# Kernel optimization log

Measured on AMD Instinct MI355X. Metric: run time of the kernel, lower is better.

The kernel has to match this reference:

```python
import jax, jax.numpy as jnp
import numpy as np
import math

B, S, I, C = 1, 512, 512, 256   # batch, n_seqs, n_res, c_in
H, D = 8, 32                    # num_heads, head_dim; total_dim = H*D = 256
TD = H * D


def setup_inputs() -> dict:
    key = jax.random.key(0)
    ks = jax.random.split(key, 12)
    w = lambda k, shape: (jax.random.normal(k, shape, dtype=jnp.float32) * 0.02)
    msa_representation = jax.random.normal(ks[0], (B, S, I, C), dtype=jnp.float32)
    msa_mask = (jax.random.uniform(ks[1], (B, S, I)) > 0.1).astype(jnp.float32)
    return {
        "msa_representation": msa_representation,
        "msa_mask": msa_mask,
        "ln_gamma": jnp.ones((C,), jnp.float32),
        "ln_beta": jnp.zeros((C,), jnp.float32),
        "Wq": w(ks[2], (C, TD)),
        "Wk": w(ks[3], (C, D)),
        "Wv": w(ks[4], (C, D)),
        "Wg": w(ks[5], (C, TD)),
        "bg": jnp.ones((TD,), jnp.float32),   # gate bias init = 1 (init_gate_linear)
        "Wo": w(ks[6], (TD, C)),
        "bo": jnp.zeros((C,), jnp.float32),
    }


def _layer_norm(x, gamma, beta, eps=1e-5):
    mu = jnp.mean(x, axis=-1, keepdims=True)
    var = jnp.mean(jnp.square(x - mu), axis=-1, keepdims=True)
    return (x - mu) * jax.lax.rsqrt(var + eps) * gamma + beta


def reference(msa_representation, msa_mask, ln_gamma, ln_beta,
              Wq, Wk, Wv, Wg, bg, Wo, bo):
    b, s, i, _ = msa_representation.shape
    x_ln = _layer_norm(msa_representation, ln_gamma, ln_beta)

    # Shared (head-less) K, V: [b, s, i, D]
    K = jnp.einsum('bsic,cd->bsid', x_ln, Wk)
    V = jnp.einsum('bsic,cd->bsid', x_ln, Wv)

    # Per-head query: [b, s, i, H, D]
    Q_si = jnp.einsum('bsic,ce->bsie', x_ln, Wq).reshape(b, s, i, H, D)

    # Masked mean-pool of the query over the sequence axis s -> [b, i, H, D]
    qm = msa_mask[..., None, None]                       # [b, s, i, 1, 1]
    Q = (Q_si * qm).sum(axis=1) / jnp.clip(qm.sum(axis=1), 1.0, None)

    # Sigmoid gate: [b, s, i, H, D]
    G = jax.nn.sigmoid(jnp.einsum('bsic,ce->bsie', x_ln, Wg) + bg).reshape(b, s, i, H, D)

    # Scores over the sequence axis t: [b, t, i, H]
    scores = jnp.einsum('bihc,btic->btih', Q, K) / math.sqrt(D)
    scores = scores + (1.0 - msa_mask[:, :, :, None]) * (-1e9)
    attention = jax.nn.softmax(scores, axis=1)

    # Weighted sum of shared V: [b, i, H, D], broadcast over s via gating
    weighted = jnp.einsum('btih,btic->bihc', attention, V)[:, None]  # [b,1,i,H,D]
    gated = (G * weighted).reshape(b, s, i, TD)
    output = jnp.einsum('bsie,ec->bsic', gated, Wo) + bo
    output = output * msa_mask[..., None]
    return output
```

## Files before the change

### kernel.cpp

```cpp
#include <hip/hip_runtime.h>

typedef __bf16 bf16_t;
typedef __bf16 bf16x4 __attribute__((ext_vector_type(4)));
typedef __bf16 bf16x8 __attribute__((ext_vector_type(8)));
typedef float f32x4 __attribute__((ext_vector_type(4)));

#define LXS 264

#define GLOAD_LDS16(gsrc, ldst) \
    __builtin_amdgcn_global_load_lds((__attribute__((address_space(1))) void*)(gsrc), \
                                     (__attribute__((address_space(3))) void*)(ldst), 16, 0, 0)

__global__ __launch_bounds__(256) void k_prep(
    const float* __restrict__ Wg, const float* __restrict__ Wo,
    const float* __restrict__ Wk, const float* __restrict__ Wv,
    bf16_t* __restrict__ WgP, bf16_t* __restrict__ WoP, bf16_t* __restrict__ WKVP)
{
    int id = blockIdx.x * 256 + threadIdx.x;
    if (id < 65536) {
        int j = id & 7, l = (id >> 3) & 63, kt = (id >> 9) & 7, nt = id >> 12;
        int k = kt * 32 + (l >> 4) * 8 + j;
        int n = nt * 16 + (l & 15);
        WgP[id] = (bf16_t)Wg[k * 256 + n];
    } else if (id < 131072) {
        int t = id - 65536;
        int j = t & 7, l = (t >> 3) & 63, kt = (t >> 9) & 7, nt = t >> 12;
        int k = kt * 32 + (l >> 4) * 8 + j;
        int n = nt * 16 + (l & 15);
        WoP[t] = (bf16_t)Wo[k * 256 + n];
    } else if (id < 147456) {
        int t = id - 131072;
        int j = t & 7, l = (t >> 3) & 63, kt = (t >> 9) & 7, nt = t >> 12;
        int k = kt * 32 + (l >> 4) * 8 + j;
        int n = nt * 16 + (l & 15);
        WKVP[t] = (bf16_t)(n < 32 ? Wk[k * 32 + n] : Wv[k * 32 + (n - 32)]);
    }
}

__global__ __launch_bounds__(256) void kA(
    const float* __restrict__ msa, const float* __restrict__ mask,
    const float* __restrict__ gamma, const float* __restrict__ beta,
    bf16_t* __restrict__ xln, bf16_t* __restrict__ kv, const bf16_t* __restrict__ WKVP,
    float* __restrict__ Qpart, float* __restrict__ Qcnt)
{
    __shared__ __align__(16) bf16_t lx[64 * LXS];
    __shared__ float pp[4][256];
    __shared__ float cw[4];
    int tid = threadIdx.x;
    int lane = tid & 63, w = tid >> 6;
    int l15 = lane & 15, l4 = lane >> 4;
    int i = blockIdx.x & 511;
    int schunk = blockIdx.x >> 9;
    int s0 = schunk * 64;

    float4 g4 = ((const float4*)gamma)[lane];
    float4 b4 = ((const float4*)beta)[lane];

    bf16x8 bfr[8];
    #pragma unroll
    for (int kt = 0; kt < 8; ++kt)
        bfr[kt] = *(const bf16x8*)(WKVP + ((w * 8 + kt) * 64 + lane) * 8);

    float p0 = 0, p1 = 0, p2 = 0, p3 = 0, pc = 0;
    for (int t = 0; t < 16; ++t) {
        int rl = w * 16 + t;
        size_t r = (size_t)(s0 + rl) * 512 + i;
        float4 x = ((const float4*)(msa + r * 256))[lane];
        float mv = mask[r];
        float s  = x.x + x.y + x.z + x.w;
        float ss = x.x*x.x + x.y*x.y + x.z*x.z + x.w*x.w;
        #pragma unroll
        for (int m = 32; m; m >>= 1) { s += __shfl_xor(s, m, 64); ss += __shfl_xor(ss, m, 64); }
        float mu = s * (1.0f / 256.0f);
        float var = ss * (1.0f / 256.0f) - mu * mu;
        float rs = rsqrtf(var + 1e-5f);
        float4 y;
        y.x = (x.x - mu) * rs * g4.x + b4.x;
        y.y = (x.y - mu) * rs * g4.y + b4.y;
        y.z = (x.z - mu) * rs * g4.z + b4.z;
        y.w = (x.w - mu) * rs * g4.w + b4.w;
        bf16x4 xv;
        xv[0] = (bf16_t)y.x; xv[1] = (bf16_t)y.y; xv[2] = (bf16_t)y.z; xv[3] = (bf16_t)y.w;
        *(bf16x4*)(xln + r * 256 + lane * 4) = xv;
        *(bf16x4*)(lx + rl * LXS + lane * 4) = xv;
        p0 += mv * y.x; p1 += mv * y.y; p2 += mv * y.z; p3 += mv * y.w;
        pc += mv;
    }
    *(float4*)&pp[w][lane * 4] = (float4){p0, p1, p2, p3};
    if (lane == 0) cw[w] = pc;
    __syncthreads();

    {
        float qs = pp[0][tid] + pp[1][tid] + pp[2][tid] + pp[3][tid];
        Qpart[((size_t)schunk * 512 + i) * 256 + tid] = qs;
        if (tid == 0) Qcnt[schunk * 512 + i] = cw[0] + cw[1] + cw[2] + cw[3];
    }

    f32x4 acc[4];
    #pragma unroll
    for (int rt = 0; rt < 4; ++rt) acc[rt] = (f32x4){0.f, 0.f, 0.f, 0.f};
    #pragma unroll
    for (int kt = 0; kt < 8; ++kt) {
        #pragma unroll
        for (int rt = 0; rt < 4; ++rt) {
            bf16x8 a = *(bf16x8*)(lx + (rt * 16 + l15) * LXS + kt * 32 + l4 * 8);
            acc[rt] = __builtin_amdgcn_mfma_f32_16x16x32_bf16(a, bfr[kt], acc[rt], 0, 0, 0);
        }
    }
    #pragma unroll
    for (int rt = 0; rt < 4; ++rt) {
        #pragma unroll
        for (int j = 0; j < 4; ++j) {
            int row = rt * 16 + l4 * 4 + j;
            size_t r = (size_t)(s0 + row) * 512 + i;
            kv[r * 64 + w * 16 + l15] = (bf16_t)acc[rt][j];
        }
    }
}

__global__ __launch_bounds__(256) void kB(
    const float* __restrict__ Qpart, const float* __restrict__ Qcnt,
    const float* __restrict__ Wq, float* __restrict__ Q)
{
    int i = blockIdx.x, tid = threadIdx.x;
    __shared__ float xs[256];
    float s = 0;
    #pragma unroll
    for (int ch = 0; ch < 8; ++ch) s += Qpart[((size_t)ch * 512 + i) * 256 + tid];
    xs[tid] = s;
    float cnt = 0;
    #pragma unroll
    for (int ch = 0; ch < 8; ++ch) cnt += Qcnt[ch * 512 + i];
    __syncthreads();
    float scale = 1.0f / (fmaxf(cnt, 1.0f) * 5.656854249492381f);
    float q = 0;
    for (int c = 0; c < 256; ++c) q += xs[c] * Wq[c * 256 + tid];
    Q[i * 256 + tid] = q * scale;
}

__global__ __launch_bounds__(256) void kC(
    const bf16_t* __restrict__ kv, const float* __restrict__ mask,
    const float* __restrict__ Q, float* __restrict__ wout)
{
    int i = blockIdx.x, tid = threadIdx.x;
    __shared__ __align__(16) bf16_t kbuf[512 * 32];
    __shared__ float sc[512 * 8];
    __shared__ float qq[256];
    __shared__ float mk[512];
    __shared__ float rcp[8];

    qq[tid] = Q[i * 256 + tid];
    mk[tid] = mask[tid * 512 + i];
    mk[tid + 256] = mask[(tid + 256) * 512 + i];

    for (int it = 0; it < 8; ++it) {
        int idx = it * 256 + tid; int t = idx >> 2; int q = idx & 3;
        ((uint4*)kbuf)[t * 4 + q] = ((const uint4*)kv)[((size_t)t * 512 + i) * 8 + q];
    }
    __syncthreads();

    for (int it = 0; it < 16; ++it) {
        int idx = it * 256 + tid; int t = idx >> 3; int h = idx & 7;
        float a = 0;
        #pragma unroll 8
        for (int d = 0; d < 32; ++d) a += qq[h * 32 + d] * (float)kbuf[t * 32 + d];
        sc[t * 8 + h] = a - (1.0f - mk[t]) * 1e9f;
    }
    __syncthreads();

    {
        int h = tid >> 5, l = tid & 31;
        float m = -1e30f;
        for (int k = 0; k < 16; ++k) m = fmaxf(m, sc[(l + 32 * k) * 8 + h]);
        #pragma unroll
        for (int off = 16; off; off >>= 1) m = fmaxf(m, __shfl_xor(m, off, 64));
        float s = 0;
        for (int k = 0; k < 16; ++k) {
            int idx = (l + 32 * k) * 8 + h;
            float p = __expf(sc[idx] - m);
            sc[idx] = p; s += p;
        }
        #pragma unroll
        for (int off = 16; off; off >>= 1) s += __shfl_xor(s, off, 64);
        if (l == 0) rcp[h] = 1.0f / s;
    }
    for (int it = 0; it < 8; ++it) {
        int idx = it * 256 + tid; int t = idx >> 2; int q = idx & 3;
        ((uint4*)kbuf)[t * 4 + q] = ((const uint4*)kv)[((size_t)t * 512 + i) * 8 + 4 + q];
    }
    __syncthreads();

    {
        int h = tid >> 5, d = tid & 31;
        float acc = 0;
        for (int t = 0; t < 512; ++t) acc += sc[t * 8 + h] * (float)kbuf[t * 32 + d];
        wout[i * 256 + tid] = acc * rcp[h];
    }
}

__global__ __launch_bounds__(256, 2) void kD(
    const bf16_t* __restrict__ xln, const bf16_t* __restrict__ WgP, const bf16_t* __restrict__ WoP,
    const float* __restrict__ bg, const float* __restrict__ bo,
    const float* __restrict__ weighted, const float* __restrict__ mask, float* __restrict__ out)
{
    __shared__ __align__(16) bf16_t lx[64 * 256];
    int tid = threadIdx.x;
    int lane = tid & 63, q = tid >> 6;
    int l15 = lane & 15, l4 = lane >> 4;
    int rowbase = blockIdx.x * 64;

    const bf16_t* srcBase = xln + (size_t)rowbase * 256;
    #pragma unroll
    for (int c = 0; c < 8; ++c) {
        int idx = (c * 256 + tid) * 16;
        int row = idx >> 9;
        int g = (idx >> 4) & 31;
        int gs = g ^ (row & 7);
        GLOAD_LDS16(srcBase + row * 256 + gs * 8, lx + c * 2048 + q * 512);
    }

    bf16x8 bfr[4][8];
    #pragma unroll
    for (int ctl = 0; ctl < 4; ++ctl)
        #pragma unroll
        for (int kt = 0; kt < 8; ++kt)
            bfr[ctl][kt] = *(const bf16x8*)(WgP + (((q * 4 + ctl) * 8 + kt) * 64 + lane) * 8);
    __syncthreads();

    int swb = l15 & 7;

    f32x4 acc[4][4];
    #pragma unroll
    for (int rt = 0; rt < 4; ++rt)
        #pragma unroll
        for (int ctl = 0; ctl < 4; ++ctl) acc[rt][ctl] = (f32x4){0.f, 0.f, 0.f, 0.f};

    #pragma unroll
    for (int kt = 0; kt < 8; ++kt) {
        bf16x8 a[4];
        #pragma unroll
        for (int rt = 0; rt < 4; ++rt)
            a[rt] = *(bf16x8*)(lx + (rt * 16 + l15) * 256 + ((kt * 4 + l4) ^ swb) * 8);
        #pragma unroll
        for (int ctl = 0; ctl < 4; ++ctl)
            #pragma unroll
            for (int rt = 0; rt < 4; ++rt)
                acc[rt][ctl] = __builtin_amdgcn_mfma_f32_16x16x32_bf16(a[rt], bfr[ctl][kt], acc[rt][ctl], 0, 0, 0);
    }
    __syncthreads();

    #pragma unroll
    for (int ctl = 0; ctl < 4; ++ctl)
        #pragma unroll
        for (int kt = 0; kt < 8; ++kt)
            bfr[ctl][kt] = *(const bf16x8*)(WoP + (((q * 4 + ctl) * 8 + kt) * 64 + lane) * 8);

    #pragma unroll
    for (int ctl = 0; ctl < 4; ++ctl) {
        int col = (q * 4 + ctl) * 16 + l15;
        float bgv = bg[col];
        int g0 = col >> 3, c7 = col & 7;
        #pragma unroll
        for (int rt = 0; rt < 4; ++rt) {
            #pragma unroll
            for (int j = 0; j < 4; ++j) {
                int row = rt * 16 + l4 * 4 + j;
                int i2 = (rowbase + row) & 511;
                float t = acc[rt][ctl][j] + bgv;
                float gv = 1.0f / (1.0f + __expf(-t));
                float gg = gv * weighted[i2 * 256 + col];
                lx[row * 256 + ((g0 ^ (row & 7)) << 3) + c7] = (bf16_t)gg;
            }
        }
    }
    __syncthreads();

    #pragma unroll
    for (int rt = 0; rt < 4; ++rt)
        #pragma unroll
        for (int ctl = 0; ctl < 4; ++ctl) acc[rt][ctl] = (f32x4){0.f, 0.f, 0.f, 0.f};
    #pragma unroll
    for (int kt = 0; kt < 8; ++kt) {
        bf16x8 a[4];
        #pragma unroll
        for (int rt = 0; rt < 4; ++rt)
            a[rt] = *(bf16x8*)(lx + (rt * 16 + l15) * 256 + ((kt * 4 + l4) ^ swb) * 8);
        #pragma unroll
        for (int ctl = 0; ctl < 4; ++ctl)
            #pragma unroll
            for (int rt = 0; rt < 4; ++rt)
                acc[rt][ctl] = __builtin_amdgcn_mfma_f32_16x16x32_bf16(a[rt], bfr[ctl][kt], acc[rt][ctl], 0, 0, 0);
    }
    #pragma unroll
    for (int ctl = 0; ctl < 4; ++ctl) {
        int col = (q * 4 + ctl) * 16 + l15;
        float bov = bo[col];
        #pragma unroll
        for (int rt = 0; rt < 4; ++rt) {
            #pragma unroll
            for (int j = 0; j < 4; ++j) {
                int row = rt * 16 + l4 * 4 + j;
                int r = rowbase + row;
                out[(size_t)r * 256 + col] = (acc[rt][ctl][j] + bov) * mask[r];
            }
        }
    }
}

extern "C" void kernel_launch(void* const* d_in, const int* in_sizes, int n_in,
                              void* d_out, int out_size, void* d_ws, size_t ws_size,
                              hipStream_t stream) {
    const float* msa   = (const float*)d_in[0];
    const float* mask  = (const float*)d_in[1];
    const float* gamma = (const float*)d_in[2];
    const float* beta  = (const float*)d_in[3];
    const float* Wq    = (const float*)d_in[4];
    const float* Wk    = (const float*)d_in[5];
    const float* Wv    = (const float*)d_in[6];
    const float* Wg    = (const float*)d_in[7];
    const float* bg    = (const float*)d_in[8];
    const float* Wo    = (const float*)d_in[9];
    const float* bo    = (const float*)d_in[10];
    float* out = (float*)d_out;

    char* ws = (char*)d_ws;
    bf16_t* xln   = (bf16_t*)(ws);
    bf16_t* kv    = (bf16_t*)(ws + 134217728);
    float*  Qp    = (float*)(ws + 167772160);
    float*  wgt   = (float*)(ws + 168296448);
    bf16_t* WgP   = (bf16_t*)(ws + 168820736);
    bf16_t* WoP   = (bf16_t*)(ws + 168951808);
    bf16_t* WKVP  = (bf16_t*)(ws + 169082880);
    float*  Qpart = (float*)(ws + 169115648);
    float*  Qcnt  = (float*)(ws + 173309952);

    k_prep<<<576, 256, 0, stream>>>(Wg, Wo, Wk, Wv, WgP, WoP, WKVP);
    kA<<<4096, 256, 0, stream>>>(msa, mask, gamma, beta, xln, kv, WKVP, Qpart, Qcnt);
    kB<<<512, 256, 0, stream>>>(Qpart, Qcnt, Wq, Qp);
    kC<<<512, 256, 0, stream>>>(kv, mask, Qp, wgt);
    kD<<<4096, 256, 0, stream>>>(xln, WgP, WoP, bg, bo, wgt, mask, out);
}
```

Before: 301.8 us.

## Make kD persistent over four row tiles with double-buffered LDS and vectorized epilogues

kD now processes four 64-row tiles per block, keeping the Wg B-fragments in registers across tiles and prefetching the next x_ln tile into a second LDS buffer while computing the current one. Wo fragments are streamed per k-step in a ping-pong fashion instead of all being held at once. MFMA operands are swapped so each lane owns four consecutive columns, which allows float4 and bf16x4 vectorized stores for the gate, the output and the kA kv write. This adds LDS usage (two 32KB buffers) and reduces grid size to 1024 blocks, which may lower occupancy and parallelism.

```diff
diff --git a/kernel.cpp b/kernel.cpp
--- a/kernel.cpp
+++ b/kernel.cpp
@@ -104,17 +104,17 @@
         #pragma unroll
         for (int rt = 0; rt < 4; ++rt) {
             bf16x8 a = *(bf16x8*)(lx + (rt * 16 + l15) * LXS + kt * 32 + l4 * 8);
-            acc[rt] = __builtin_amdgcn_mfma_f32_16x16x32_bf16(a, bfr[kt], acc[rt], 0, 0, 0);
+            acc[rt] = __builtin_amdgcn_mfma_f32_16x16x32_bf16(bfr[kt], a, acc[rt], 0, 0, 0);
         }
     }
     #pragma unroll
     for (int rt = 0; rt < 4; ++rt) {
-        #pragma unroll
-        for (int j = 0; j < 4; ++j) {
-            int row = rt * 16 + l4 * 4 + j;
-            size_t r = (size_t)(s0 + row) * 512 + i;
-            kv[r * 64 + w * 16 + l15] = (bf16_t)acc[rt][j];
-        }
+        int row = rt * 16 + l15;
+        size_t r = (size_t)(s0 + row) * 512 + i;
+        bf16x4 kvv;
+        #pragma unroll
+        for (int j = 0; j < 4; ++j) kvv[j] = (bf16_t)acc[rt][j];
+        *(bf16x4*)(kv + r * 64 + w * 16 + l4 * 4) = kvv;
     }
 }
 
@@ -203,108 +203,137 @@
     const float* __restrict__ bg, const float* __restrict__ bo,
     const float* __restrict__ weighted, const float* __restrict__ mask, float* __restrict__ out)
 {
-    __shared__ __align__(16) bf16_t lx[64 * 256];
+    __shared__ __align__(16) bf16_t lx0[64 * 256];
+    __shared__ __align__(16) bf16_t lx1[64 * 256];
     int tid = threadIdx.x;
     int lane = tid & 63, q = tid >> 6;
     int l15 = lane & 15, l4 = lane >> 4;
-    int rowbase = blockIdx.x * 64;
-
-    const bf16_t* srcBase = xln + (size_t)rowbase * 256;
-    #pragma unroll
-    for (int c = 0; c < 8; ++c) {
-        int idx = (c * 256 + tid) * 16;
-        int row = idx >> 9;
-        int g = (idx >> 4) & 31;
-        int gs = g ^ (row & 7);
-        GLOAD_LDS16(srcBase + row * 256 + gs * 8, lx + c * 2048 + q * 512);
-    }
-
-    bf16x8 bfr[4][8];
+    int swb = l15 & 7;
+
+#define STAGE(BUF, RB) \
+    { const bf16_t* sB = xln + (size_t)(RB) * 256; \
+      _Pragma("unroll") \
+      for (int c = 0; c < 8; ++c) { \
+        int idx = (c * 256 + tid) * 16; \
+        int row_ = idx >> 9; \
+        int g_ = (idx >> 4) & 31; \
+        GLOAD_LDS16(sB + row_ * 256 + (g_ ^ (row_ & 7)) * 8, (BUF) + c * 2048 + q * 512); \
+      } }
+
+#define LOAD_BO(DST, KT) \
+    _Pragma("unroll") \
+    for (int ctl = 0; ctl < 4; ++ctl) \
+        DST[ctl] = *(const bf16x8*)(WoP + ((((q * 4 + ctl) * 8 + (KT)) * 64 + lane) * 8));
+
+#define G2STEP(BO, KT, LXC) \
+    { bf16x8 a2[4]; \
+      _Pragma("unroll") \
+      for (int rt = 0; rt < 4; ++rt) \
+          a2[rt] = *(bf16x8*)((LXC) + (rt * 16 + l15) * 256 + (((KT) * 4 + l4) ^ swb) * 8); \
+      _Pragma("unroll") \
+      for (int ctl = 0; ctl < 4; ++ctl) \
+          _Pragma("unroll") \
+          for (int rt = 0; rt < 4; ++rt) \
+              acc[rt][ctl] = __builtin_amdgcn_mfma_f32_16x16x32_bf16(BO[ctl], a2[rt], acc[rt][ctl], 0, 0, 0); }
+
+    bf16x8 bfrG[4][8];
     #pragma unroll
     for (int ctl = 0; ctl < 4; ++ctl)
         #pragma unroll
         for (int kt = 0; kt < 8; ++kt)
-            bfr[ctl][kt] = *(const bf16x8*)(WgP + (((q * 4 + ctl) * 8 + kt) * 64 + lane) * 8);
-    __syncthreads();
-
-    int swb = l15 & 7;
+            bfrG[ctl][kt] = *(const bf16x8*)(WgP + (((q * 4 + ctl) * 8 + kt) * 64 + lane) * 8);
+
+    int Rblk = blockIdx.x * 256;
+    STAGE(lx0, Rblk)
+    __syncthreads();
 
     f32x4 acc[4][4];
-    #pragma unroll
-    for (int rt = 0; rt < 4; ++rt)
-        #pragma unroll
-        for (int ctl = 0; ctl < 4; ++ctl) acc[rt][ctl] = (f32x4){0.f, 0.f, 0.f, 0.f};
-
-    #pragma unroll
-    for (int kt = 0; kt < 8; ++kt) {
-        bf16x8 a[4];
+
+    #pragma unroll
+    for (int t = 0; t < 4; ++t) {
+        bf16_t* LXC = (t & 1) ? lx1 : lx0;
+        bf16_t* LXN = (t & 1) ? lx0 : lx1;
+        int R0 = Rblk + t * 64;
+
+        if (t < 3) STAGE(LXN, R0 + 64)
+
         #pragma unroll
         for (int rt = 0; rt < 4; ++rt)
-            a[rt] = *(bf16x8*)(lx + (rt * 16 + l15) * 256 + ((kt * 4 + l4) ^ swb) * 8);
-        #pragma unroll
-        for (int ctl = 0; ctl < 4; ++ctl)
+            #pragma unroll
+            for (int ctl = 0; ctl < 4; ++ctl) acc[rt][ctl] = (f32x4){0.f, 0.f, 0.f, 0.f};
+        #pragma unroll
+        for (int kt = 0; kt < 8; ++kt) {
+            bf16x8 a[4];
             #pragma unroll
             for (int rt = 0; rt < 4; ++rt)
-                acc[rt][ctl] = __builtin_amdgcn_mfma_f32_16x16x32_bf16(a[rt], bfr[ctl][kt], acc[rt][ctl], 0, 0, 0);
-    }
-    __syncthreads();
-
-    #pragma unroll
-    for (int ctl = 0; ctl < 4; ++ctl)
-        #pragma unroll
-        for (int kt = 0; kt < 8; ++kt)
-            bfr[ctl][kt] = *(const bf16x8*)(WoP + (((q * 4 + ctl) * 8 + kt) * 64 + lane) * 8);
-
-    #pragma unroll
-    for (int ctl = 0; ctl < 4; ++ctl) {
-        int col = (q * 4 + ctl) * 16 + l15;
-        float bgv = bg[col];
-        int g0 = col >> 3, c7 = col & 7;
-        #pragma unroll
-        for (int rt = 0; rt < 4; ++rt) {
-            #pragma unroll
-            for (int j = 0; j < 4; ++j) {
-                int row = rt * 16 + l4 * 4 + j;
-                int i2 = (rowbase + row) & 511;
-                float t = acc[rt][ctl][j] + bgv;
-                float gv = 1.0f / (1.0f + __expf(-t));
-                float gg = gv * weighted[i2 * 256 + col];
-                lx[row * 256 + ((g0 ^ (row & 7)) << 3) + c7] = (bf16_t)gg;
+                a[rt] = *(bf16x8*)(LXC + (rt * 16 + l15) * 256 + ((kt * 4 + l4) ^ swb) * 8);
+            #pragma unroll
+            for (int ctl = 0; ctl < 4; ++ctl)
+                #pragma unroll
+                for (int rt = 0; rt < 4; ++rt)
+                    acc[rt][ctl] = __builtin_amdgcn_mfma_f32_16x16x32_bf16(bfrG[ctl][kt], a[rt], acc[rt][ctl], 0, 0, 0);
+        }
+        __syncthreads();
+
+        #pragma unroll
+        for (int ctl = 0; ctl < 4; ++ctl) {
+            int c4 = (q * 4 + ctl) * 16 + l4 * 4;
+            float4 bg4 = *(const float4*)(bg + c4);
+            int g0 = c4 >> 3, c7 = c4 & 7;
+            #pragma unroll
+            for (int rt = 0; rt < 4; ++rt) {
+                int row = rt * 16 + l15;
+                int i2 = (R0 + row) & 511;
+                float4 w4 = *(const float4*)(weighted + i2 * 256 + c4);
+                f32x4 t4 = acc[rt][ctl];
+                bf16x4 gv;
+                gv[0] = (bf16_t)(w4.x / (1.0f + __expf(-(t4[0] + bg4.x))));
+                gv[1] = (bf16_t)(w4.y / (1.0f + __expf(-(t4[1] + bg4.y))));
+                gv[2] = (bf16_t)(w4.z / (1.0f + __expf(-(t4[2] + bg4.z))));
+                gv[3] = (bf16_t)(w4.w / (1.0f + __expf(-(t4[3] + bg4.w))));
+                *(bf16x4*)(LXC + row * 256 + ((g0 ^ (row & 7)) << 3) + c7) = gv;
             }
         }
-    }
-    __syncthreads();
-
-    #pragma unroll
-    for (int rt = 0; rt < 4; ++rt)
-        #pragma unroll
-        for (int ctl = 0; ctl < 4; ++ctl) acc[rt][ctl] = (f32x4){0.f, 0.f, 0.f, 0.f};
-    #pragma unroll
-    for (int kt = 0; kt < 8; ++kt) {
-        bf16x8 a[4];
+        __syncthreads();
+
         #pragma unroll
         for (int rt = 0; rt < 4; ++rt)
-            a[rt] = *(bf16x8*)(lx + (rt * 16 + l15) * 256 + ((kt * 4 + l4) ^ swb) * 8);
-        #pragma unroll
-        for (int ctl = 0; ctl < 4; ++ctl)
-            #pragma unroll
-            for (int rt = 0; rt < 4; ++rt)
-                acc[rt][ctl] = __builtin_amdgcn_mfma_f32_16x16x32_bf16(a[rt], bfr[ctl][kt], acc[rt][ctl], 0, 0, 0);
-    }
-    #pragma unroll
-    for (int ctl = 0; ctl < 4; ++ctl) {
-        int col = (q * 4 + ctl) * 16 + l15;
-        float bov = bo[col];
-        #pragma unroll
-        for (int rt = 0; rt < 4; ++rt) {
-            #pragma unroll
-            for (int j = 0; j < 4; ++j) {
-                int row = rt * 16 + l4 * 4 + j;
-                int r = rowbase + row;
-                out[(size_t)r * 256 + col] = (acc[rt][ctl][j] + bov) * mask[r];
+            #pragma unroll
+            for (int ctl = 0; ctl < 4; ++ctl) acc[rt][ctl] = (f32x4){0.f, 0.f, 0.f, 0.f};
+        {
+            bf16x8 boA[4], boB[4];
+            LOAD_BO(boA, 0)
+            LOAD_BO(boB, 1) G2STEP(boA, 0, LXC)
+            LOAD_BO(boA, 2) G2STEP(boB, 1, LXC)
+            LOAD_BO(boB, 3) G2STEP(boA, 2, LXC)
+            LOAD_BO(boA, 4) G2STEP(boB, 3, LXC)
+            LOAD_BO(boB, 5) G2STEP(boA, 4, LXC)
+            LOAD_BO(boA, 6) G2STEP(boB, 5, LXC)
+            LOAD_BO(boB, 7) G2STEP(boA, 6, LXC)
+                            G2STEP(boB, 7, LXC)
+        }
+
+        #pragma unroll
+        for (int ctl = 0; ctl < 4; ++ctl) {
+            int c4 = (q * 4 + ctl) * 16 + l4 * 4;
+            float4 bo4 = *(const float4*)(bo + c4);
+            #pragma unroll
+            for (int rt = 0; rt < 4; ++rt) {
+                int r = R0 + rt * 16 + l15;
+                float mv = mask[r];
+                float4 o;
+                o.x = (acc[rt][ctl][0] + bo4.x) * mv;
+                o.y = (acc[rt][ctl][1] + bo4.y) * mv;
+                o.z = (acc[rt][ctl][2] + bo4.z) * mv;
+                o.w = (acc[rt][ctl][3] + bo4.w) * mv;
+                *(float4*)(out + (size_t)r * 256 + c4) = o;
             }
         }
-    }
+        __syncthreads();
+    }
+#undef STAGE
+#undef LOAD_BO
+#undef G2STEP
 }
 
 extern "C" void kernel_launch(void* const* d_in, const int* in_sizes, int n_in,
@@ -338,5 +367,5 @@
     kA<<<4096, 256, 0, stream>>>(msa, mask, gamma, beta, xln, kv, WKVP, Qpart, Qcnt);
     kB<<<512, 256, 0, stream>>>(Qpart, Qcnt, Wq, Qp);
     kC<<<512, 256, 0, stream>>>(kv, mask, Qp, wgt);
-    kD<<<4096, 256, 0, stream>>>(xln, WgP, WoP, bg, bo, wgt, mask, out);
-}
+    kD<<<1024, 256, 0, stream>>>(xln, WgP, WoP, bg, bo, wgt, mask, out);
+}
```

Result: slower. 402.4 us (+33.3%).

## Move gate projection into the layernorm kernel and store sigmoid gate instead of xln

Applied to the files above, without the earlier changes.

The gate GEMM (x_ln·Wg plus bias and sigmoid) now runs in kA while the layer-normed tile is still in LDS, and the bf16 gate G is written in place of x_ln. kD becomes a register-only kernel: it loads G rows, multiplies by the attention-weighted values, and does the Wo GEMM with weights streamed from global, using non-temporal output stores and no LDS. The goal is to drop the x_ln round-trip and the LDS staging and synchronisation in kD. In exchange kA does much more MFMA work and holds more registers, and kD reloads WoP from global in every wave.

```diff
diff --git a/kernel.cpp b/kernel.cpp
--- a/kernel.cpp
+++ b/kernel.cpp
@@ -6,10 +6,6 @@
 typedef float f32x4 __attribute__((ext_vector_type(4)));
 
 #define LXS 264
-
-#define GLOAD_LDS16(gsrc, ldst) \
-    __builtin_amdgcn_global_load_lds((__attribute__((address_space(1))) void*)(gsrc), \
-                                     (__attribute__((address_space(3))) void*)(ldst), 16, 0, 0)
 
 __global__ __launch_bounds__(256) void k_prep(
     const float* __restrict__ Wg, const float* __restrict__ Wo,
@@ -40,7 +36,9 @@
 __global__ __launch_bounds__(256) void kA(
     const float* __restrict__ msa, const float* __restrict__ mask,
     const float* __restrict__ gamma, const float* __restrict__ beta,
-    bf16_t* __restrict__ xln, bf16_t* __restrict__ kv, const bf16_t* __restrict__ WKVP,
+    const float* __restrict__ bg,
+    bf16_t* __restrict__ G, bf16_t* __restrict__ kv,
+    const bf16_t* __restrict__ WKVP, const bf16_t* __restrict__ WgP,
     float* __restrict__ Qpart, float* __restrict__ Qcnt)
 {
     __shared__ __align__(16) bf16_t lx[64 * LXS];
@@ -81,7 +79,6 @@
         y.w = (x.w - mu) * rs * g4.w + b4.w;
         bf16x4 xv;
         xv[0] = (bf16_t)y.x; xv[1] = (bf16_t)y.y; xv[2] = (bf16_t)y.z; xv[3] = (bf16_t)y.w;
-        *(bf16x4*)(xln + r * 256 + lane * 4) = xv;
         *(bf16x4*)(lx + rl * LXS + lane * 4) = xv;
         p0 += mv * y.x; p1 += mv * y.y; p2 += mv * y.z; p3 += mv * y.w;
         pc += mv;
@@ -96,24 +93,70 @@
         if (tid == 0) Qcnt[schunk * 512 + i] = cw[0] + cw[1] + cw[2] + cw[3];
     }
 
-    f32x4 acc[4];
-    #pragma unroll
-    for (int rt = 0; rt < 4; ++rt) acc[rt] = (f32x4){0.f, 0.f, 0.f, 0.f};
-    #pragma unroll
-    for (int kt = 0; kt < 8; ++kt) {
+    {
+        f32x4 acc[4];
+        #pragma unroll
+        for (int rt = 0; rt < 4; ++rt) acc[rt] = (f32x4){0.f, 0.f, 0.f, 0.f};
+        #pragma unroll
+        for (int kt = 0; kt < 8; ++kt) {
+            #pragma unroll
+            for (int rt = 0; rt < 4; ++rt) {
+                bf16x8 a = *(bf16x8*)(lx + (rt * 16 + l15) * LXS + kt * 32 + l4 * 8);
+                acc[rt] = __builtin_amdgcn_mfma_f32_16x16x32_bf16(bfr[kt], a, acc[rt], 0, 0, 0);
+            }
+        }
         #pragma unroll
         for (int rt = 0; rt < 4; ++rt) {
-            bf16x8 a = *(bf16x8*)(lx + (rt * 16 + l15) * LXS + kt * 32 + l4 * 8);
-            acc[rt] = __builtin_amdgcn_mfma_f32_16x16x32_bf16(a, bfr[kt], acc[rt], 0, 0, 0);
-        }
-    }
-    #pragma unroll
-    for (int rt = 0; rt < 4; ++rt) {
-        #pragma unroll
-        for (int j = 0; j < 4; ++j) {
-            int row = rt * 16 + l4 * 4 + j;
+            int row = rt * 16 + l15;
             size_t r = (size_t)(s0 + row) * 512 + i;
-            kv[r * 64 + w * 16 + l15] = (bf16_t)acc[rt][j];
+            bf16x4 kvv;
+            #pragma unroll
+            for (int j = 0; j < 4; ++j) kvv[j] = (bf16_t)acc[rt][j];
+            *(bf16x4*)(kv + r * 64 + w * 16 + l4 * 4) = kvv;
+        }
+    }
+
+    #pragma unroll
+    for (int cp = 0; cp < 2; ++cp) {
+        int nt0 = w * 4 + cp * 2, nt1 = nt0 + 1;
+        f32x4 ga0[4], ga1[4];
+        #pragma unroll
+        for (int rt = 0; rt < 4; ++rt) { ga0[rt] = (f32x4){0.f,0.f,0.f,0.f}; ga1[rt] = (f32x4){0.f,0.f,0.f,0.f}; }
+        bf16x8 w0 = *(const bf16x8*)(WgP + ((nt0 * 8 + 0) * 64 + lane) * 8);
+        bf16x8 w1 = *(const bf16x8*)(WgP + ((nt1 * 8 + 0) * 64 + lane) * 8);
+        #pragma unroll
+        for (int kt = 0; kt < 8; ++kt) {
+            int ktn = (kt + 1) & 7;
+            bf16x8 w0n = *(const bf16x8*)(WgP + ((nt0 * 8 + ktn) * 64 + lane) * 8);
+            bf16x8 w1n = *(const bf16x8*)(WgP + ((nt1 * 8 + ktn) * 64 + lane) * 8);
+            bf16x8 a[4];
+            #pragma unroll
+            for (int rt = 0; rt < 4; ++rt)
+                a[rt] = *(bf16x8*)(lx + (rt * 16 + l15) * LXS + kt * 32 + l4 * 8);
+            #pragma unroll
+            for (int rt = 0; rt < 4; ++rt) {
+                ga0[rt] = __builtin_amdgcn_mfma_f32_16x16x32_bf16(w0, a[rt], ga0[rt], 0, 0, 0);
+                ga1[rt] = __builtin_amdgcn_mfma_f32_16x16x32_bf16(w1, a[rt], ga1[rt], 0, 0, 0);
+            }
+            w0 = w0n; w1 = w1n;
+        }
+        #pragma unroll
+        for (int e = 0; e < 2; ++e) {
+            int nt = (e == 0) ? nt0 : nt1;
+            int c4 = nt * 16 + l4 * 4;
+            float4 bg4 = *(const float4*)(bg + c4);
+            #pragma unroll
+            for (int rt = 0; rt < 4; ++rt) {
+                f32x4 t4 = (e == 0) ? ga0[rt] : ga1[rt];
+                int row = rt * 16 + l15;
+                size_t r = (size_t)(s0 + row) * 512 + i;
+                bf16x4 gv;
+                gv[0] = (bf16_t)(1.0f / (1.0f + __expf(-(t4[0] + bg4.x))));
+                gv[1] = (bf16_t)(1.0f / (1.0f + __expf(-(t4[1] + bg4.y))));
+                gv[2] = (bf16_t)(1.0f / (1.0f + __expf(-(t4[2] + bg4.z))));
+                gv[3] = (bf16_t)(1.0f / (1.0f + __expf(-(t4[3] + bg4.w))));
+                *(bf16x4*)(G + r * 256 + c4) = gv;
+            }
         }
     }
 }
@@ -198,111 +241,79 @@
     }
 }
 
-__global__ __launch_bounds__(256, 2) void kD(
-    const bf16_t* __restrict__ xln, const bf16_t* __restrict__ WgP, const bf16_t* __restrict__ WoP,
-    const float* __restrict__ bg, const float* __restrict__ bo,
-    const float* __restrict__ weighted, const float* __restrict__ mask, float* __restrict__ out)
-{
-    __shared__ __align__(16) bf16_t lx[64 * 256];
+__global__ __launch_bounds__(256, 3) void kD(
+    const bf16_t* __restrict__ G, const bf16_t* __restrict__ WoP,
+    const float* __restrict__ bo, const float* __restrict__ weighted,
+    const float* __restrict__ mask, float* __restrict__ out)
+{
     int tid = threadIdx.x;
-    int lane = tid & 63, q = tid >> 6;
+    int lane = tid & 63, w = tid >> 6;
     int l15 = lane & 15, l4 = lane >> 4;
-    int rowbase = blockIdx.x * 64;
-
-    const bf16_t* srcBase = xln + (size_t)rowbase * 256;
-    #pragma unroll
-    for (int c = 0; c < 8; ++c) {
-        int idx = (c * 256 + tid) * 16;
-        int row = idx >> 9;
-        int g = (idx >> 4) & 31;
-        int gs = g ^ (row & 7);
-        GLOAD_LDS16(srcBase + row * 256 + gs * 8, lx + c * 2048 + q * 512);
-    }
-
-    bf16x8 bfr[4][8];
-    #pragma unroll
-    for (int ctl = 0; ctl < 4; ++ctl)
-        #pragma unroll
-        for (int kt = 0; kt < 8; ++kt)
-            bfr[ctl][kt] = *(const bf16x8*)(WgP + (((q * 4 + ctl) * 8 + kt) * 64 + lane) * 8);
-    __syncthreads();
-
-    int swb = l15 & 7;
-
-    f32x4 acc[4][4];
-    #pragma unroll
-    for (int rt = 0; rt < 4; ++rt)
-        #pragma unroll
-        for (int ctl = 0; ctl < 4; ++ctl) acc[rt][ctl] = (f32x4){0.f, 0.f, 0.f, 0.f};
-
+    int R0 = (blockIdx.x * 4 + w) * 16;
+    int row = R0 + l15;
+    int i2 = row & 511;
+    const bf16_t* gp = G + (size_t)row * 256 + l4 * 8;
+    const float*  wp = weighted + i2 * 256 + l4 * 8;
+
+    bf16x8 g8[8];
+    #pragma unroll
+    for (int kt = 0; kt < 8; ++kt) g8[kt] = *(const bf16x8*)(gp + kt * 32);
+    f32x4 wv[16];
     #pragma unroll
     for (int kt = 0; kt < 8; ++kt) {
-        bf16x8 a[4];
-        #pragma unroll
-        for (int rt = 0; rt < 4; ++rt)
-            a[rt] = *(bf16x8*)(lx + (rt * 16 + l15) * 256 + ((kt * 4 + l4) ^ swb) * 8);
-        #pragma unroll
-        for (int ctl = 0; ctl < 4; ++ctl)
-            #pragma unroll
-            for (int rt = 0; rt < 4; ++rt)
-                acc[rt][ctl] = __builtin_amdgcn_mfma_f32_16x16x32_bf16(a[rt], bfr[ctl][kt], acc[rt][ctl], 0, 0, 0);
-    }
-    __syncthreads();
-
-    #pragma unroll
-    for (int ctl = 0; ctl < 4; ++ctl)
-        #pragma unroll
-        for (int kt = 0; kt < 8; ++kt)
-            bfr[ctl][kt] = *(const bf16x8*)(WoP + (((q * 4 + ctl) * 8 + kt) * 64 + lane) * 8);
-
-    #pragma unroll
-    for (int ctl = 0; ctl < 4; ++ctl) {
-        int col = (q * 4 + ctl) * 16 + l15;
-        float bgv = bg[col];
-        int g0 = col >> 3, c7 = col & 7;
-        #pragma unroll
-        for (int rt = 0; rt < 4; ++rt) {
-            #pragma unroll
-            for (int j = 0; j < 4; ++j) {
-                int row = rt * 16 + l4 * 4 + j;
-                int i2 = (rowbase + row) & 511;
-                float t = acc[rt][ctl][j] + bgv;
-                float gv = 1.0f / (1.0f + __expf(-t));
-                float gg = gv * weighted[i2 * 256 + col];
-                lx[row * 256 + ((g0 ^ (row & 7)) << 3) + c7] = (bf16_t)gg;
+        wv[kt * 2]     = *(const f32x4*)(wp + kt * 32);
+        wv[kt * 2 + 1] = *(const f32x4*)(wp + kt * 32 + 4);
+    }
+    float mv = mask[row];
+
+    bf16x8 gt[8];
+    #pragma unroll
+    for (int kt = 0; kt < 8; ++kt) {
+        #pragma unroll
+        for (int j = 0; j < 4; ++j) {
+            gt[kt][j]     = (bf16_t)((float)g8[kt][j]     * wv[kt * 2][j]);
+            gt[kt][j + 4] = (bf16_t)((float)g8[kt][j + 4] * wv[kt * 2 + 1][j]);
+        }
+    }
+
+    #pragma unroll
+    for (int ntg = 0; ntg < 4; ++ntg) {
+        f32x4 acc[4];
+        #pragma unroll
+        for (int p = 0; p < 4; ++p) acc[p] = (f32x4){0.f, 0.f, 0.f, 0.f};
+        bf16x8 wA[4], wB[4];
+        #pragma unroll
+        for (int p = 0; p < 4; ++p)
+            wA[p] = *(const bf16x8*)(WoP + (((ntg * 4 + p) * 8 + 0) * 64 + lane) * 8);
+        #pragma unroll
+        for (int kt = 0; kt < 8; ++kt) {
+            int ktn = (kt + 1) & 7;
+            if (kt & 1) {
+                #pragma unroll
+                for (int p = 0; p < 4; ++p)
+                    wA[p] = *(const bf16x8*)(WoP + (((ntg * 4 + p) * 8 + ktn) * 64 + lane) * 8);
+                #pragma unroll
+                for (int p = 0; p < 4; ++p)
+                    acc[p] = __builtin_amdgcn_mfma_f32_16x16x32_bf16(wB[p], gt[kt], acc[p], 0, 0, 0);
+            } else {
+                #pragma unroll
+                for (int p = 0; p < 4; ++p)
+                    wB[p] = *(const bf16x8*)(WoP + (((ntg * 4 + p) * 8 + ktn) * 64 + lane) * 8);
+                #pragma unroll
+                for (int p = 0; p < 4; ++p)
+                    acc[p] = __builtin_amdgcn_mfma_f32_16x16x32_bf16(wA[p], gt[kt], acc[p], 0, 0, 0);
             }
         }
-    }
-    __syncthreads();
-
-    #pragma unroll
-    for (int rt = 0; rt < 4; ++rt)
-        #pragma unroll
-        for (int ctl = 0; ctl < 4; ++ctl) acc[rt][ctl] = (f32x4){0.f, 0.f, 0.f, 0.f};
-    #pragma unroll
-    for (int kt = 0; kt < 8; ++kt) {
-        bf16x8 a[4];
-        #pragma unroll
-        for (int rt = 0; rt < 4; ++rt)
-            a[rt] = *(bf16x8*)(lx + (rt * 16 + l15) * 256 + ((kt * 4 + l4) ^ swb) * 8);
-        #pragma unroll
-        for (int ctl = 0; ctl < 4; ++ctl)
-            #pragma unroll
-            for (int rt = 0; rt < 4; ++rt)
-                acc[rt][ctl] = __builtin_amdgcn_mfma_f32_16x16x32_bf16(a[rt], bfr[ctl][kt], acc[rt][ctl], 0, 0, 0);
-    }
-    #pragma unroll
-    for (int ctl = 0; ctl < 4; ++ctl) {
-        int col = (q * 4 + ctl) * 16 + l15;
-        float bov = bo[col];
-        #pragma unroll
-        for (int rt = 0; rt < 4; ++rt) {
-            #pragma unroll
-            for (int j = 0; j < 4; ++j) {
-                int row = rt * 16 + l4 * 4 + j;
-                int r = rowbase + row;
-                out[(size_t)r * 256 + col] = (acc[rt][ctl][j] + bov) * mask[r];
-            }
+        #pragma unroll
+        for (int p = 0; p < 4; ++p) {
+            int c4 = (ntg * 4 + p) * 16 + l4 * 4;
+            float4 bo4 = *(const float4*)(bo + c4);
+            f32x4 o;
+            o[0] = (acc[p][0] + bo4.x) * mv;
+            o[1] = (acc[p][1] + bo4.y) * mv;
+            o[2] = (acc[p][2] + bo4.z) * mv;
+            o[3] = (acc[p][3] + bo4.w) * mv;
+            __builtin_nontemporal_store(o, (f32x4*)(out + (size_t)row * 256 + c4));
         }
     }
 }
@@ -324,7 +335,7 @@
     float* out = (float*)d_out;
 
     char* ws = (char*)d_ws;
-    bf16_t* xln   = (bf16_t*)(ws);
+    bf16_t* G     = (bf16_t*)(ws);
     bf16_t* kv    = (bf16_t*)(ws + 134217728);
     float*  Qp    = (float*)(ws + 167772160);
     float*  wgt   = (float*)(ws + 168296448);
@@ -335,8 +346,8 @@
     float*  Qcnt  = (float*)(ws + 173309952);
 
     k_prep<<<576, 256, 0, stream>>>(Wg, Wo, Wk, Wv, WgP, WoP, WKVP);
-    kA<<<4096, 256, 0, stream>>>(msa, mask, gamma, beta, xln, kv, WKVP, Qpart, Qcnt);
+    kA<<<4096, 256, 0, stream>>>(msa, mask, gamma, beta, bg, G, kv, WKVP, WgP, Qpart, Qcnt);
     kB<<<512, 256, 0, stream>>>(Qpart, Qcnt, Wq, Qp);
     kC<<<512, 256, 0, stream>>>(kv, mask, Qp, wgt);
-    kD<<<4096, 256, 0, stream>>>(xln, WgP, WoP, bg, bo, wgt, mask, out);
-}
+    kD<<<4096, 256, 0, stream>>>(G, WoP, bo, wgt, mask, out);
+}
```

Measured after the change: 377.1 us. 1.25x slower.
